# Kernel optimization log

Measured on AMD Instinct MI355X. Metric: run time of the kernel, lower is better.

The kernel has to match this reference:

```python
import jax, jax.numpy as jnp
import numpy as np

N = 50000          # n_nodes
E_RAND = 800000    # random edges (before self-loops)
D_FEAT = 128
ALPHA = 0.1
NITER = 10


def setup_inputs() -> dict:
    key = jax.random.key(0)
    k1, k2, k3 = jax.random.split(key, 3)
    r = jax.random.randint(k1, (E_RAND,), 0, N)
    c = jax.random.randint(k2, (E_RAND,), 0, N)
    loop = jnp.arange(N)
    # A + I  (self-loops appended, matching calc_A_hat's sp.eye addition)
    rows = jnp.concatenate([r, loop]).astype(jnp.int32)   # [850000]
    cols = jnp.concatenate([c, loop]).astype(jnp.int32)   # [850000]
    # D_vec = row sums of (A + I); symmetric normalization D^-1/2 (A+I) D^-1/2
    deg = jax.ops.segment_sum(jnp.ones(rows.shape[0], jnp.float32), rows, num_segments=N)
    dinv = 1.0 / jnp.sqrt(jnp.maximum(deg, 1.0))
    # A_hat values pre-scaled by (1 - alpha), as registered in the buffer
    vals = ((1.0 - ALPHA) * dinv[rows] * dinv[cols]).astype(jnp.float32)
    E = jax.random.normal(k3, (N, D_FEAT), dtype=jnp.float32)
    return {"E": E, "rows": rows, "cols": cols, "vals": vals}


def reference(E, rows, cols, vals):
    # preds_{t+1} = A_hat @ preds_t + alpha * E   (niter power-iteration steps)
    # spmm via gather + segment_sum over the COO edge list.
    def step(preds, _):
        msg = vals[:, None] * preds[cols]                       # [nnz, d]
        preds = jax.ops.segment_sum(msg, rows, num_segments=N) + ALPHA * E
        return preds, None
    out, _ = jax.lax.scan(step, E, None, length=NITER)
    return out
```

## Files before the change

kernel.cpp:

```cpp
#include <hip/hip_runtime.h>


#define ALPHA 0.1f
#define NITER 10
#define DFEAT 128
#define CHUNK 1024
#define EPB   4096


__global__ void hist_rows(const int* __restrict__ rows, int* __restrict__ counts, int nnz) {
    int e = blockIdx.x * blockDim.x + threadIdx.x;
    if (e < nnz) atomicAdd(&counts[rows[e]], 1);
}

__global__ void scan_reduce(const int* __restrict__ counts, int* __restrict__ blockSums, int N) {
    __shared__ int lds[256];
    int b = blockIdx.x, t = threadIdx.x;
    int base = b * CHUNK + t * 4;
    int s = 0;
    if (base + 4 <= N) {
        int4 v = *(const int4*)(counts + base);
        s = v.x + v.y + v.z + v.w;
    } else {
        for (int k = 0; k < 4; ++k) if (base + k < N) s += counts[base + k];
    }
    lds[t] = s;
    __syncthreads();
    for (int off = 128; off > 0; off >>= 1) {
        if (t < off) lds[t] += lds[t + off];
        __syncthreads();
    }
    if (t == 0) blockSums[b] = lds[0];
}

__global__ void scan_blocksums(const int* __restrict__ blockSums, int* __restrict__ blockOff,
                               int* __restrict__ rowptr, int NB, int N) {
    __shared__ int lds[1024];
    int t = threadIdx.x;
    int v = (t < NB) ? blockSums[t] : 0;
    lds[t] = v;
    __syncthreads();
    for (int off = 1; off < 1024; off <<= 1) {
        int u = (t >= off) ? lds[t - off] : 0;
        __syncthreads();
        lds[t] += u;
        __syncthreads();
    }
    if (t < NB) blockOff[t] = (t == 0) ? 0 : lds[t - 1];
    if (t == 1023) rowptr[N] = lds[1023];
}

__global__ void scan_write(const int* __restrict__ counts, const int* __restrict__ blockOff,
                           int* __restrict__ rowptr, int* __restrict__ bucketCursor, int N) {
    __shared__ int lds[256];
    int b = blockIdx.x, t = threadIdx.x;
    int base = b * CHUNK + t * 4;
    int c0 = 0, c1 = 0, c2 = 0, c3 = 0;
    if (base + 4 <= N) {
        int4 v = *(const int4*)(counts + base);
        c0 = v.x; c1 = v.y; c2 = v.z; c3 = v.w;
    } else {
        if (base + 0 < N) c0 = counts[base + 0];
        if (base + 1 < N) c1 = counts[base + 1];
        if (base + 2 < N) c2 = counts[base + 2];
        if (base + 3 < N) c3 = counts[base + 3];
    }
    int s = c0 + c1 + c2 + c3;
    lds[t] = s;
    __syncthreads();
    for (int off = 1; off < 256; off <<= 1) {
        int u = (t >= off) ? lds[t - off] : 0;
        __syncthreads();
        lds[t] += u;
        __syncthreads();
    }
    int run = ((t == 0) ? 0 : lds[t - 1]) + blockOff[b];
    #pragma unroll
    for (int k = 0; k < 4; ++k) {
        int r = base + k;
        if (r < N) {
            rowptr[r] = run;
            if ((r & 255) == 0) bucketCursor[r >> 8] = run;
            run += (k == 0 ? c0 : k == 1 ? c1 : k == 2 ? c2 : c3);
        }
    }
}

__global__ void csr_bucketA(const int* __restrict__ rows, const int* __restrict__ cols,
                            const float* __restrict__ vals, int* __restrict__ bucketCursor,
                            int2* __restrict__ staging, int nnz, int nbuck) {
    __shared__ int h[256], base[256], cur[256];
    const int t = threadIdx.x;
    const int e0 = blockIdx.x * EPB;

    if (t < 256) { h[t] = 0; cur[t] = 0; }
    __syncthreads();

    #pragma unroll
    for (int k = 0; k < EPB / 256; ++k) {
        int idx = e0 + k * 256 + t;
        if (idx < nnz) atomicAdd(&h[rows[idx] >> 8], 1);
    }
    __syncthreads();

    if (t < 256 && t < nbuck && h[t] > 0)
        base[t] = atomicAdd(&bucketCursor[t], h[t]);
    __syncthreads();

    #pragma unroll
    for (int k = 0; k < EPB / 256; ++k) {
        int idx = e0 + k * 256 + t;
        if (idx < nnz) {
            int r = rows[idx];
            int b = r >> 8;
            int o = atomicAdd(&cur[b], 1);
            int2 p;
            p.x = (cols[idx] << 8) | (r & 255);
            p.y = __float_as_int(vals[idx]);
            staging[base[b] + o] = p;
        }
    }
}

__global__ void csr_bucketB(const int* __restrict__ rowptr, const int2* __restrict__ staging,
                            int2* __restrict__ packed, int N) {
    __shared__ int cur[256];
    const int b = blockIdx.x;
    const int t = threadIdx.x;
    const int r0 = b << 8;

    int rlim = r0 + t;
    cur[t] = rowptr[rlim < N ? rlim : N];
    __syncthreads();

    const int s0 = rowptr[r0];
    int r1 = r0 + 256;
    const int s1 = rowptr[r1 < N ? r1 : N];

    for (int idx = s0 + t; idx < s1; idx += 256) {
        int2 e = staging[idx];
        int rl = e.x & 255;
        int pos = atomicAdd(&cur[rl], 1);
        int2 p;
        p.x = e.x & 0xffffff00;
        p.y = e.y;
        packed[pos] = p;
    }
}


__device__ inline unsigned f32_to_bf16_rne(float f) {
    unsigned x = __float_as_uint(f);
    return (x + 0x7fffu + ((x >> 16) & 1u)) >> 16;
}

__global__ void cvt_f32_bf16(const float2* __restrict__ in, unsigned* __restrict__ out, int n2) {
    int i = blockIdx.x * blockDim.x + threadIdx.x;
    if (i < n2) {
        float2 v = in[i];
        out[i] = f32_to_bf16_rne(v.x) | (f32_to_bf16_rne(v.y) << 16);
    }
}


#define GACC(cofs, vbits)                                                         \
    {   uint4 x = *(const uint4*)(srcb + (size_t)(unsigned)(cofs) + soff);        \
        float v = __int_as_float(vbits);                                          \
        acc[0] += v * __uint_as_float(x.x << 16);                                 \
        acc[1] += v * __uint_as_float(x.x & 0xffff0000u);                         \
        acc[2] += v * __uint_as_float(x.y << 16);                                 \
        acc[3] += v * __uint_as_float(x.y & 0xffff0000u);                         \
        acc[4] += v * __uint_as_float(x.z << 16);                                 \
        acc[5] += v * __uint_as_float(x.z & 0xffff0000u);                         \
        acc[6] += v * __uint_as_float(x.w << 16);                                 \
        acc[7] += v * __uint_as_float(x.w & 0xffff0000u); }

template <bool DSTB>
__global__ void spmm_quad(const int* __restrict__ rowptr, const int2* __restrict__ packed,
                          const char* __restrict__ srcb, const char* __restrict__ Eb,
                          const float* __restrict__ Ef, void* __restrict__ dst, int N) {
    int wave = (blockIdx.x * blockDim.x + threadIdx.x) >> 6;
    int nwav = (gridDim.x * blockDim.x) >> 6;
    int lane = threadIdx.x & 63;
    int g    = lane >> 4;
    int sub  = lane & 15;
    const size_t soff = (size_t)sub * 16;

    for (int w4 = wave * 4; w4 < N; w4 += nwav * 4) {
        int w = w4 + g;
        if (w >= N) w = N - 1;
        bool valid = (w4 + g < N);

        int s = rowptr[w];
        int e = rowptr[w + 1];

        float acc[8];
        if constexpr (DSTB) {
            uint4 ev = *(const uint4*)(Eb + (size_t)w * 256 + soff);
            acc[0] = ALPHA * __uint_as_float(ev.x << 16);
            acc[1] = ALPHA * __uint_as_float(ev.x & 0xffff0000u);
            acc[2] = ALPHA * __uint_as_float(ev.y << 16);
            acc[3] = ALPHA * __uint_as_float(ev.y & 0xffff0000u);
            acc[4] = ALPHA * __uint_as_float(ev.z << 16);
            acc[5] = ALPHA * __uint_as_float(ev.z & 0xffff0000u);
            acc[6] = ALPHA * __uint_as_float(ev.w << 16);
            acc[7] = ALPHA * __uint_as_float(ev.w & 0xffff0000u);
        } else {
            const float4* ep = (const float4*)(Ef + (size_t)w * DFEAT + sub * 8);
            float4 e0 = ep[0], e1 = ep[1];
            acc[0] = ALPHA * e0.x; acc[1] = ALPHA * e0.y;
            acc[2] = ALPHA * e0.z; acc[3] = ALPHA * e0.w;
            acc[4] = ALPHA * e1.x; acc[5] = ALPHA * e1.y;
            acc[6] = ALPHA * e1.z; acc[7] = ALPHA * e1.w;
        }

        int i = s;
        if (i < e && (i & 1)) {
            int2 p = packed[i];
            GACC(p.x, p.y)
            ++i;
        }
        for (; i + 4 <= e; i += 4) {
            int4 q0 = *(const int4*)(packed + i);
            int4 q1 = *(const int4*)(packed + i + 2);
            GACC(q0.x, q0.y)
            GACC(q0.z, q0.w)
            GACC(q1.x, q1.y)
            GACC(q1.z, q1.w)
        }
        for (; i < e; ++i) {
            int2 p = packed[i];
            GACC(p.x, p.y)
        }

        if (valid) {
            if constexpr (DSTB) {
                uint4 o;
                o.x = f32_to_bf16_rne(acc[0]) | (f32_to_bf16_rne(acc[1]) << 16);
                o.y = f32_to_bf16_rne(acc[2]) | (f32_to_bf16_rne(acc[3]) << 16);
                o.z = f32_to_bf16_rne(acc[4]) | (f32_to_bf16_rne(acc[5]) << 16);
                o.w = f32_to_bf16_rne(acc[6]) | (f32_to_bf16_rne(acc[7]) << 16);
                *(uint4*)((char*)dst + (size_t)w * 256 + soff) = o;
            } else {
                float4* op = (float4*)((float*)dst + (size_t)w * DFEAT + sub * 8);
                op[0] = make_float4(acc[0], acc[1], acc[2], acc[3]);
                op[1] = make_float4(acc[4], acc[5], acc[6], acc[7]);
            }
        }
    }
}

#undef GACC

extern "C" void kernel_launch(void* const* d_in, const int* in_sizes, int n_in,
                              void* d_out, int out_size, void* d_ws, size_t ws_size,
                              hipStream_t stream) {
    const float* E    = (const float*)d_in[0];
    const int*   rows = (const int*)d_in[1];
    const int*   cols = (const int*)d_in[2];
    const float* vals = (const float*)d_in[3];
    float*       out  = (float*)d_out;

    const int nd  = in_sizes[0];
    const int nnz = in_sizes[1];
    const int N   = nd / DFEAT;
    const int NB  = (N + CHUNK - 1) / CHUNK;
    const int nbuck = (N + 255) >> 8;

    const int Np  = (N + 4 + 3) & ~3;
    const int NBp = (NB + 3) & ~3;
    char* ws = (char*)d_ws;
    char*  bufA    = ws;
    char*  bufB    = ws + (size_t)nd * 2;
    int*   rowptr  = (int*)(ws + (size_t)nd * 4);
    int*   bcur    = rowptr + Np;
    int*   bsums   = bcur + Np;
    int*   boff    = bsums + NBp;
    size_t pk_off  = (((size_t)nd * 4 + (size_t)(2 * Np + 2 * NBp) * 4) + 15) & ~(size_t)15;
    int2*  packed  = (int2*)(ws + pk_off);
    int2*  staging = (int2*)bufA;

    char* Eb = (char*)d_out;

    dim3 blk(256);
    dim3 gE((nnz + 255) / 256);

    hipMemsetAsync(bcur, 0, (size_t)N * 4, stream);
    hist_rows<<<gE, blk, 0, stream>>>(rows, bcur, nnz);
    scan_reduce<<<NB, 256, 0, stream>>>(bcur, bsums, N);
    scan_blocksums<<<1, 1024, 0, stream>>>(bsums, boff, rowptr, NB, N);
    scan_write<<<NB, 256, 0, stream>>>(bcur, boff, rowptr, bcur, N);
    csr_bucketA<<<(nnz + EPB - 1) / EPB, blk, 0, stream>>>(rows, cols, vals, bcur,
                                                           staging, nnz, nbuck);
    csr_bucketB<<<nbuck, blk, 0, stream>>>(rowptr, staging, packed, N);

    const int n2 = nd / 2;
    cvt_f32_bf16<<<(n2 + 255) / 256, blk, 0, stream>>>((const float2*)E, (unsigned*)Eb, n2);

    int quads  = (N + 3) / 4;
    int waves  = (quads + 1) / 2;
    int blocks = (waves + 3) / 4;
    dim3 gS(blocks);

    char* cur = Eb;
    char* nxt = bufA;
    for (int it = 1; it <= NITER - 1; ++it) {
        spmm_quad<true><<<gS, blk, 0, stream>>>(rowptr, packed, cur, Eb, E, nxt, N);
        cur = nxt;
        nxt = (cur == bufA) ? bufB : bufA;
    }
    spmm_quad<false><<<gS, blk, 0, stream>>>(rowptr, packed, cur, Eb, E, out, N);
}
```

Baseline: 416.6 us.

## Sort rows by degree so each wave processes similar-length rows

Adds a degree counting sort (histogram, scan, scatter) that builds a permutation of rows grouped by out-degree. The SpMM kernel then takes its rows through this permutation, so the four rows sharing a wave have similar nonzero counts and lanes idle less. In exchange it adds three small setup kernels, an extra indirection per row, and scattered output writes and E reads, which reduce locality.

```diff
diff --git a/kernel.cpp b/kernel.cpp
--- a/kernel.cpp
+++ b/kernel.cpp
@@ -149,6 +149,34 @@
 }
 
 
+__global__ void deg_hist(const int* __restrict__ rowptr, int* __restrict__ dhist, int N) {
+    int r = blockIdx.x * blockDim.x + threadIdx.x;
+    if (r < N) {
+        int d = rowptr[r + 1] - rowptr[r];
+        if (d > 63) d = 63;
+        atomicAdd(&dhist[d], 1);
+    }
+}
+
+__global__ void deg_scan(const int* __restrict__ dhist, int* __restrict__ dcur) {
+    if (threadIdx.x == 0) {
+        int run = 0;
+        for (int i = 0; i < 64; ++i) { int c = dhist[i]; dcur[i] = run; run += c; }
+    }
+}
+
+__global__ void deg_scatter(const int* __restrict__ rowptr, int* __restrict__ dcur,
+                            int* __restrict__ perm, int N) {
+    int r = blockIdx.x * blockDim.x + threadIdx.x;
+    if (r < N) {
+        int d = rowptr[r + 1] - rowptr[r];
+        if (d > 63) d = 63;
+        int pos = atomicAdd(&dcur[d], 1);
+        perm[pos] = r;
+    }
+}
+
+
 __device__ inline unsigned f32_to_bf16_rne(float f) {
     unsigned x = __float_as_uint(f);
     return (x + 0x7fffu + ((x >> 16) & 1u)) >> 16;
@@ -176,7 +204,8 @@
         acc[7] += v * __uint_as_float(x.w & 0xffff0000u); }
 
 template <bool DSTB>
-__global__ void spmm_quad(const int* __restrict__ rowptr, const int2* __restrict__ packed,
+__global__ void spmm_quad(const int* __restrict__ rowptr, const int* __restrict__ perm,
+                          const int2* __restrict__ packed,
                           const char* __restrict__ srcb, const char* __restrict__ Eb,
                           const float* __restrict__ Ef, void* __restrict__ dst, int N) {
     int wave = (blockIdx.x * blockDim.x + threadIdx.x) >> 6;
@@ -187,9 +216,10 @@
     const size_t soff = (size_t)sub * 16;
 
     for (int w4 = wave * 4; w4 < N; w4 += nwav * 4) {
-        int w = w4 + g;
-        if (w >= N) w = N - 1;
-        bool valid = (w4 + g < N);
+        int wi = w4 + g;
+        bool valid = (wi < N);
+        if (!valid) wi = N - 1;
+        int w = perm[wi];
 
         int s = rowptr[w];
         int e = rowptr[w + 1];
@@ -274,9 +304,12 @@
     char*  bufB    = ws + (size_t)nd * 2;
     int*   rowptr  = (int*)(ws + (size_t)nd * 4);
     int*   bcur    = rowptr + Np;
-    int*   bsums   = bcur + Np;
+    int*   perm    = bcur + Np;
+    int*   bsums   = perm + Np;
     int*   boff    = bsums + NBp;
-    size_t pk_off  = (((size_t)nd * 4 + (size_t)(2 * Np + 2 * NBp) * 4) + 15) & ~(size_t)15;
+    int*   dhist   = boff + NBp;
+    int*   dcur    = dhist + 64;
+    size_t pk_off  = (((size_t)nd * 4 + (size_t)(3 * Np + 2 * NBp + 128) * 4) + 15) & ~(size_t)15;
     int2*  packed  = (int2*)(ws + pk_off);
     int2*  staging = (int2*)bufA;
 
@@ -284,8 +317,10 @@
 
     dim3 blk(256);
     dim3 gE((nnz + 255) / 256);
+    dim3 gN((N + 255) / 256);
 
     hipMemsetAsync(bcur, 0, (size_t)N * 4, stream);
+    hipMemsetAsync(dhist, 0, 64 * 4, stream);
     hist_rows<<<gE, blk, 0, stream>>>(rows, bcur, nnz);
     scan_reduce<<<NB, 256, 0, stream>>>(bcur, bsums, N);
     scan_blocksums<<<1, 1024, 0, stream>>>(bsums, boff, rowptr, NB, N);
@@ -294,6 +329,10 @@
                                                            staging, nnz, nbuck);
     csr_bucketB<<<nbuck, blk, 0, stream>>>(rowptr, staging, packed, N);
 
+    deg_hist<<<gN, blk, 0, stream>>>(rowptr, dhist, N);
+    deg_scan<<<1, 64, 0, stream>>>(dhist, dcur);
+    deg_scatter<<<gN, blk, 0, stream>>>(rowptr, dcur, perm, N);
+
     const int n2 = nd / 2;
     cvt_f32_bf16<<<(n2 + 255) / 256, blk, 0, stream>>>((const float2*)E, (unsigned*)Eb, n2);
 
@@ -305,9 +344,9 @@
     char* cur = Eb;
     char* nxt = bufA;
     for (int it = 1; it <= NITER - 1; ++it) {
-        spmm_quad<true><<<gS, blk, 0, stream>>>(rowptr, packed, cur, Eb, E, nxt, N);
+        spmm_quad<true><<<gS, blk, 0, stream>>>(rowptr, perm, packed, cur, Eb, E, nxt, N);
         cur = nxt;
         nxt = (cur == bufA) ? bufB : bufA;
     }
-    spmm_quad<false><<<gS, blk, 0, stream>>>(rowptr, packed, cur, Eb, E, out, N);
-}
+    spmm_quad<false><<<gS, blk, 0, stream>>>(rowptr, perm, packed, cur, Eb, E, out, N);
+}
```

Measured after the change: 719.9 us. 72.8% more time.
